# Performance work log

Measured on AMD Instinct MI355X. Metric: run time of the kernel, lower is better.

Reference implementation:

```python
import math
import jax, jax.numpy as jnp
import numpy as np

B, S, E, A, H, L, V = 4, 1024, 1024, 64, 16, 2, 32000
EPS = 1e-5
SCALE = math.sqrt(E)  # torch code scales by sqrt(input_dim) = sqrt(embedding_dim)
W_INIT_SCALE = 0.05   # torch.rand is U[0,1); scaled down for numerically sane softmax


def setup_inputs() -> dict:
    key = jax.random.key(0)
    ks = jax.random.split(key, 6)
    return {
        "x": jax.random.randint(ks[0], (B, S), 0, V),
        "emb": jax.random.normal(ks[1], (V, E), dtype=jnp.float32) * 0.02,
        "ln_gamma": jnp.ones((L, E), dtype=jnp.float32),
        "ln_beta": jnp.zeros((L, E), dtype=jnp.float32),
        "Wq": jax.random.uniform(ks[2], (L, H, A, E), dtype=jnp.float32) * W_INIT_SCALE,
        "Wk": jax.random.uniform(ks[3], (L, H, A, E), dtype=jnp.float32) * W_INIT_SCALE,
        "Wv": jax.random.uniform(ks[4], (L, H, E, E), dtype=jnp.float32) * W_INIT_SCALE,
    }


def _attn_layer(h, gamma, beta, wq, wk, wv):
    # h: [B,H,S,E]; LayerNorm over last dim (biased variance, like torch)
    mu = jnp.mean(h, axis=-1, keepdims=True)
    var = jnp.mean(jnp.square(h - mu), axis=-1, keepdims=True)
    hn = (h - mu) * jax.lax.rsqrt(var + EPS) * gamma + beta
    q = jnp.einsum('bhse,hae->bhsa', hn, wq)   # [B,H,S,A]
    k = jnp.einsum('bhse,hae->bhsa', hn, wk)   # [B,H,S,A]
    v = jnp.einsum('bhse,hoe->bhso', hn, wv)   # [B,H,S,E]
    scores = jnp.einsum('bhsa,bhta->bhst', q, k) / SCALE  # [B,H,S,S]
    w = jax.nn.softmax(scores, axis=-1)
    return jnp.einsum('bhst,bhto->bhso', w, v)  # [B,H,S,E]


def reference(x, emb, ln_gamma, ln_beta, Wq, Wk, Wv):
    # embed then replicate across heads: [B,S,E] -> [B,H,S,E]
    h = jnp.broadcast_to(emb[x][:, None, :, :], (B, H, S, E))
    for l in range(L):
        h = _attn_layer(h, ln_gamma[l], ln_beta[l], Wq[l], Wk[l], Wv[l])
    return h
```

## Files before the change

### kernel.cpp

```cpp
#include <hip/hip_runtime.h>

#define B_ 4
#define S_ 1024
#define E_ 1024
#define A_ 64
#define H_ 16
#define L_ 2

static constexpr float LN_EPS = 1e-5f;
static constexpr float INV_SCALE = 1.0f / 32.0f;

typedef __attribute__((ext_vector_type(8))) short bf16x8;
typedef __attribute__((ext_vector_type(4))) float f32x4;

__device__ __forceinline__ unsigned short f2bf(float f) {
  unsigned u = __float_as_uint(f);
  u += 0x7fffu + ((u >> 16) & 1u);
  return (unsigned short)(u >> 16);
}
__device__ __forceinline__ float bf2f(unsigned short s) {
  return __uint_as_float(((unsigned)s) << 16);
}

__device__ __forceinline__ float block_sum256(float v, float* red) {
#pragma unroll
  for (int o = 32; o > 0; o >>= 1) v += __shfl_down(v, o, 64);
  const int lane = threadIdx.x & 63;
  const int w = threadIdx.x >> 6;
  if (lane == 0) red[w] = v;
  __syncthreads();
  if (threadIdx.x == 0) red[0] = red[0] + red[1] + red[2] + red[3];
  __syncthreads();
  float r = red[0];
  __syncthreads();
  return r;
}

__device__ __forceinline__ float block_max256(float v, float* red) {
#pragma unroll
  for (int o = 32; o > 0; o >>= 1) v = fmaxf(v, __shfl_down(v, o, 64));
  const int lane = threadIdx.x & 63;
  const int w = threadIdx.x >> 6;
  if (lane == 0) red[w] = v;
  __syncthreads();
  if (threadIdx.x == 0) red[0] = fmaxf(fmaxf(red[0], red[1]), fmaxf(red[2], red[3]));
  __syncthreads();
  float r = red[0];
  __syncthreads();
  return r;
}

__global__ __launch_bounds__(256) void cvt_f32_bf16(const float* __restrict__ in,
                                                    unsigned short* __restrict__ out, long n) {
  long i = ((long)blockIdx.x * 256 + threadIdx.x) * 4;
  const long stride = (long)gridDim.x * 1024;
  for (; i < n; i += stride) {
    float4 v = *(const float4*)(in + i);
    ushort4 o;
    o.x = f2bf(v.x); o.y = f2bf(v.y); o.z = f2bf(v.z); o.w = f2bf(v.w);
    *(ushort4*)(out + i) = o;
  }
}

__global__ __launch_bounds__(256) void cvt_qk_concat(const float* __restrict__ Wq,
                                                     const float* __restrict__ Wk,
                                                     unsigned short* __restrict__ out) {
  const long total = (long)L_ * H_ * 128 * E_;
  long i = ((long)blockIdx.x * 256 + threadIdx.x) * 4;
  const long stride = (long)gridDim.x * 1024;
  for (; i < total; i += stride) {
    const long e = i % E_;
    const long rowhe = i / E_;
    const int row = (int)(rowhe % 128);
    const long lh = rowhe / 128;
    const float* src = (row < 64 ? Wq : Wk) + (lh * 64 + (row & 63)) * E_ + e;
    float4 v = *(const float4*)src;
    ushort4 o;
    o.x = f2bf(v.x); o.y = f2bf(v.y); o.z = f2bf(v.z); o.w = f2bf(v.w);
    *(ushort4*)(out + i) = o;
  }
}

__global__ __launch_bounds__(256) void embed_ln_kernel(
    const int* __restrict__ x, const float* __restrict__ emb,
    const float* __restrict__ gamma, const float* __restrict__ beta,
    unsigned short* __restrict__ out) {
  __shared__ float red[4];
  const int row = blockIdx.x;
  const int tid = threadIdx.x;
  const float* src = emb + (long)x[row] * E_;
  float4 v = *(const float4*)(src + tid * 4);
  const float mean = block_sum256(v.x + v.y + v.z + v.w, red) * (1.f / E_);
  float dx = v.x - mean, dy = v.y - mean, dz = v.z - mean, dw = v.w - mean;
  const float var = block_sum256(dx * dx + dy * dy + dz * dz + dw * dw, red) * (1.f / E_);
  const float rstd = rsqrtf(var + LN_EPS);
  float4 g = *(const float4*)(gamma + tid * 4);
  float4 b = *(const float4*)(beta + tid * 4);
  ushort4 o;
  o.x = f2bf(dx * rstd * g.x + b.x);
  o.y = f2bf(dy * rstd * g.y + b.y);
  o.z = f2bf(dz * rstd * g.z + b.z);
  o.w = f2bf(dw * rstd * g.w + b.w);
  *(ushort4*)(out + (long)row * E_ + tid * 4) = o;
}

__global__ __launch_bounds__(256) void ln_bf16_kernel(
    const unsigned short* __restrict__ h, const float* __restrict__ gamma,
    const float* __restrict__ beta, unsigned short* __restrict__ out) {
  __shared__ float red[4];
  const long row = blockIdx.x;
  const int tid = threadIdx.x;
  ushort4 raw = *(const ushort4*)(h + row * (long)E_ + tid * 4);
  float vx = bf2f(raw.x), vy = bf2f(raw.y), vz = bf2f(raw.z), vw = bf2f(raw.w);
  const float mean = block_sum256(vx + vy + vz + vw, red) * (1.f / E_);
  float dx = vx - mean, dy = vy - mean, dz = vz - mean, dw = vw - mean;
  const float var = block_sum256(dx * dx + dy * dy + dz * dz + dw * dw, red) * (1.f / E_);
  const float rstd = rsqrtf(var + LN_EPS);
  float4 g = *(const float4*)(gamma + tid * 4);
  float4 b = *(const float4*)(beta + tid * 4);
  ushort4 o;
  o.x = f2bf(dx * rstd * g.x + b.x);
  o.y = f2bf(dy * rstd * g.y + b.y);
  o.z = f2bf(dz * rstd * g.z + b.z);
  o.w = f2bf(dw * rstd * g.w + b.w);
  *(ushort4*)(out + row * E_ + tid * 4) = o;
}

__global__ __launch_bounds__(256) void softmax_bf16_kernel(unsigned short* __restrict__ sc) {
  __shared__ float red[4];
  unsigned short* p = sc + (long)blockIdx.x * S_;
  const int tid = threadIdx.x;
  ushort4 raw = *(const ushort4*)(p + tid * 4);
  float v0 = bf2f(raw.x), v1 = bf2f(raw.y), v2 = bf2f(raw.z), v3 = bf2f(raw.w);
  float m = block_max256(fmaxf(fmaxf(v0, v1), fmaxf(v2, v3)), red);
  v0 = __expf(v0 - m); v1 = __expf(v1 - m); v2 = __expf(v2 - m); v3 = __expf(v3 - m);
  const float s = block_sum256(v0 + v1 + v2 + v3, red);
  const float inv = 1.f / s;
  ushort4 o;
  o.x = f2bf(v0 * inv); o.y = f2bf(v1 * inv); o.z = f2bf(v2 * inv); o.w = f2bf(v3 * inv);
  *(ushort4*)(p + tid * 4) = o;
}

__device__ __forceinline__ void gload_lds16(const void* g, void* l) {
  __builtin_amdgcn_global_load_lds((const __attribute__((address_space(1))) void*)g,
                                   (__attribute__((address_space(3))) void*)l, 16, 0, 0);
}

template <int ROWS>
__device__ __forceinline__ void stage_tile(const unsigned short* __restrict__ src, int ldRow,
                                           unsigned short* lds, int tid) {
  const int rb = tid >> 3;
  const int gslot = (tid & 7) ^ (rb & 7);
  const int wbase = (tid >> 6) * 512;
#pragma unroll
  for (int i = 0; i < ROWS / 32; ++i) {
    const unsigned short* g = src + (long)(i * 32 + rb) * ldRow + gslot * 8;
    gload_lds16(g, lds + i * 2048 + wbase);
  }
}

__device__ __forceinline__ bf16x8 lds_frag(const unsigned short* base, int r, int slot) {
  const int byteoff = (r << 7) + ((slot ^ (r & 7)) << 4);
  return *(const bf16x8*)((const char*)base + byteoff);
}

template <int BM, int BN, bool OUT_BF16>
__global__ __launch_bounds__(256) void mfma_gemm_nt(
    const unsigned short* __restrict__ Aall, const unsigned short* __restrict__ Ball,
    void* __restrict__ Call, int M, int N, int K, int lda, int ldb,
    long aSB, long aSH, long bSB, long bSH, int Hn, float alpha) {
  __shared__ unsigned short As[BM * 64];
  __shared__ unsigned short Bs[BN * 64];
  const int batch = blockIdx.z;
  const int bb = batch / Hn, hh = batch % Hn;
  const unsigned short* Ap = Aall + (long)bb * aSB + (long)hh * aSH;
  const unsigned short* Bp = Ball + (long)bb * bSB + (long)hh * bSH;
  const int tid = threadIdx.x;
  const int lane = tid & 63;
  const int wave = tid >> 6;
  const int wr = wave >> 1, wc = wave & 1;
  const int bm = blockIdx.x * BM, bn = blockIdx.y * BN;
  constexpr int FM = BM / 32, FN = BN / 32;

  f32x4 acc[FM][FN];
#pragma unroll
  for (int i = 0; i < FM; ++i)
#pragma unroll
    for (int j = 0; j < FN; ++j) acc[i][j] = (f32x4)(0.f);

  for (int k0 = 0; k0 < K; k0 += 64) {
    stage_tile<BM>(Ap + (long)bm * lda + k0, lda, As, tid);
    stage_tile<BN>(Bp + (long)bn * ldb + k0, ldb, Bs, tid);
    __syncthreads();
#pragma unroll
    for (int kb = 0; kb < 2; ++kb) {
      const int slot = (kb << 2) + (lane >> 4);
      bf16x8 af[FM], bfv[FN];
#pragma unroll
      for (int mi = 0; mi < FM; ++mi)
        af[mi] = lds_frag(As, wr * (BM / 2) + mi * 16 + (lane & 15), slot);
#pragma unroll
      for (int ni = 0; ni < FN; ++ni)
        bfv[ni] = lds_frag(Bs, wc * (BN / 2) + ni * 16 + (lane & 15), slot);
#pragma unroll
      for (int mi = 0; mi < FM; ++mi)
#pragma unroll
        for (int ni = 0; ni < FN; ++ni)
          acc[mi][ni] = __builtin_amdgcn_mfma_f32_16x16x32_bf16(af[mi], bfv[ni], acc[mi][ni], 0, 0, 0);
    }
    __syncthreads();
  }

#pragma unroll
  for (int mi = 0; mi < FM; ++mi) {
    const int row = bm + wr * (BM / 2) + mi * 16 + ((lane >> 4) << 2);
#pragma unroll
    for (int ni = 0; ni < FN; ++ni) {
      const int col = bn + wc * (BN / 2) + ni * 16 + (lane & 15);
#pragma unroll
      for (int r = 0; r < 4; ++r) {
        const float v = acc[mi][ni][r] * alpha;
        const long idx = (long)batch * M * N + (long)(row + r) * N + col;
        if constexpr (OUT_BF16)
          ((unsigned short*)Call)[idx] = f2bf(v);
        else
          ((float*)Call)[idx] = v;
      }
    }
  }
}

__device__ __forceinline__ void stage_unit256(const unsigned short* __restrict__ src, int ldRow,
                                              char* lds_unit, int tid) {
#pragma unroll
  for (int i = 0; i < 2; ++i) {
    const int r = i * 128 + (tid >> 2);
    const int sg = (tid & 3) ^ ((r >> 1) & 3);
    const unsigned short* g = src + (long)r * ldRow + sg * 8;
    gload_lds16(g, lds_unit + i * 8192 + ((tid >> 6) << 10));
  }
}

__device__ __forceinline__ bf16x8 lds_frag256(const char* opbase, int kh, int r, int ss) {
  return *(const bf16x8*)(opbase + kh * 16384 + r * 64 + ((ss ^ ((r >> 1) & 3)) << 4));
}

template <bool OUT_BF16>
__global__ __launch_bounds__(512, 2) void mfma_gemm256_nt(
    const unsigned short* __restrict__ Aall, const unsigned short* __restrict__ Ball,
    void* __restrict__ Call, int M, int N, int K, int lda, int ldb,
    long aSB, long aSH, long bSB, long bSH, int Hn, float alpha) {
  extern __shared__ char lds[];
  const int nx = gridDim.x, ny = gridDim.y;
  const int nwg = nx * ny * gridDim.z;
  int f = blockIdx.x + nx * (blockIdx.y + ny * blockIdx.z);
  if ((nwg & 7) == 0) f = (f & 7) * (nwg >> 3) + (f >> 3);
  const int bx = f % nx;
  const int by = (f / nx) % ny;
  const int batch = f / (nx * ny);

  const int bb = batch / Hn, hh = batch % Hn;
  const unsigned short* Ap = Aall + (long)bb * aSB + (long)hh * aSH + (long)bx * 256 * lda;
  const unsigned short* Bp = Ball + (long)bb * bSB + (long)hh * bSH + (long)by * 256 * ldb;
  const int tid = threadIdx.x;
  const int lane = tid & 63;
  const int w = tid >> 6;
  const int wr = w >> 2, wc = w & 3;

  f32x4 acc[8][4];
#pragma unroll
  for (int i = 0; i < 8; ++i)
#pragma unroll
    for (int j = 0; j < 4; ++j) acc[i][j] = (f32x4)(0.f);

  const int NT = K >> 6;
  stage_unit256(Ap, lda, lds, tid);
  stage_unit256(Bp, ldb, lds + 32768, tid);
  stage_unit256(Ap + 32, lda, lds + 16384, tid);
  stage_unit256(Bp + 32, ldb, lds + 32768 + 16384, tid);
  asm volatile("s_waitcnt vmcnt(0)\n\ts_barrier" ::: "memory");

  for (int t = 0; t < NT; ++t) {
    const char* cur = lds + (t & 1) * 65536;
    char* nxt = lds + ((t + 1) & 1) * 65536;
    const unsigned short* An = Ap + (long)(t + 1) * 64;
    const unsigned short* Bn = Bp + (long)(t + 1) * 64;
    const bool pf = (t + 1 < NT);
#pragma unroll
    for (int kh = 0; kh < 2; ++kh) {
      bf16x8 a[8], b[4];
      const int ss = lane >> 4;
#pragma unroll
      for (int mi = 0; mi < 8; ++mi)
        a[mi] = lds_frag256(cur, kh, wr * 128 + mi * 16 + (lane & 15), ss);
#pragma unroll
      for (int ni = 0; ni < 4; ++ni)
        b[ni] = lds_frag256(cur + 32768, kh, wc * 64 + ni * 16 + (lane & 15), ss);
      if (pf) {
        stage_unit256(An + kh * 32, lda, nxt + kh * 16384, tid);
        stage_unit256(Bn + kh * 32, ldb, nxt + 32768 + kh * 16384, tid);
      }
      asm volatile("s_barrier" ::: "memory");
      __builtin_amdgcn_s_setprio(1);
#pragma unroll
      for (int mi = 0; mi < 8; ++mi)
#pragma unroll
        for (int ni = 0; ni < 4; ++ni)
          acc[mi][ni] = __builtin_amdgcn_mfma_f32_16x16x32_bf16(a[mi], b[ni], acc[mi][ni], 0, 0, 0);
      __builtin_amdgcn_s_setprio(0);
      asm volatile("s_waitcnt vmcnt(4)\n\ts_barrier" ::: "memory");
    }
  }

#pragma unroll
  for (int mi = 0; mi < 8; ++mi) {
    const int row0 = bx * 256 + wr * 128 + mi * 16 + ((lane >> 4) << 2);
#pragma unroll
    for (int ni = 0; ni < 4; ++ni) {
      const int col = by * 256 + wc * 64 + ni * 16 + (lane & 15);
#pragma unroll
      for (int r = 0; r < 4; ++r) {
        const float v = acc[mi][ni][r] * alpha;
        const long idx = (long)batch * M * N + (long)(row0 + r) * N + col;
        if constexpr (OUT_BF16)
          ((unsigned short*)Call)[idx] = f2bf(v);
        else
          ((float*)Call)[idx] = v;
      }
    }
  }
}

extern "C" void kernel_launch(void* const* d_in, const int* in_sizes, int n_in,
                              void* d_out, int out_size, void* d_ws, size_t ws_size,
                              hipStream_t stream) {
  const int* x = (const int*)d_in[0];
  const float* emb = (const float*)d_in[1];
  const float* gamma = (const float*)d_in[2];
  const float* beta = (const float*)d_in[3];
  const float* Wq = (const float*)d_in[4];
  const float* Wk = (const float*)d_in[5];
  const float* Wv = (const float*)d_in[6];
  float* out = (float*)d_out;

  (void)hipFuncSetAttribute(reinterpret_cast<const void*>(&mfma_gemm256_nt<true>),
                            hipFuncAttributeMaxDynamicSharedMemorySize, 131072);
  (void)hipFuncSetAttribute(reinterpret_cast<const void*>(&mfma_gemm256_nt<false>),
                            hipFuncAttributeMaxDynamicSharedMemorySize, 131072);

  const long WQK_N = (long)L_ * H_ * 128 * E_;
  const long WV_N = (long)L_ * H_ * E_ * E_;
  const long HN_N = (long)B_ * H_ * S_ * E_;
  const long QK_N = (long)B_ * H_ * S_ * 128;
  unsigned short* wqk = (unsigned short*)d_ws;
  unsigned short* wv_bf = wqk + WQK_N;
  unsigned short* hn = wv_bf + WV_N;
  unsigned short* qk = hn + HN_N;
  unsigned short* v_t = qk + QK_N;
  unsigned short* sc = v_t + HN_N;
  unsigned short* hid0 = (unsigned short*)d_out;

  const dim3 blk(256), blk512(512);
  const dim3 grid256(4, 4, 64);
  cvt_qk_concat<<<2048, blk, 0, stream>>>(Wq, Wk, wqk);
  cvt_f32_bf16<<<4096, blk, 0, stream>>>(Wv, wv_bf, WV_N);

  for (int l = 0; l < L_; ++l) {
    long hSB, hSH;
    if (l == 0) {
      embed_ln_kernel<<<B_ * S_, blk, 0, stream>>>(x, emb, gamma, beta, hn);
      hSB = (long)S_ * E_; hSH = 0;
    } else {
      ln_bf16_kernel<<<B_ * H_ * S_, blk, 0, stream>>>(
          hid0, gamma + (long)l * E_, beta + (long)l * E_, hn);
      hSB = (long)H_ * S_ * E_; hSH = (long)S_ * E_;
    }
    mfma_gemm_nt<128, 128, true><<<dim3(8, 1, 64), blk, 0, stream>>>(
        hn, wqk + (long)l * H_ * 128 * E_, qk, S_, 128, E_, E_, E_,
        hSB, hSH, 0L, (long)128 * E_, H_, 1.f);
    mfma_gemm256_nt<true><<<grid256, blk512, 131072, stream>>>(
        wv_bf + (long)l * H_ * E_ * E_, hn, v_t, E_, S_, E_, E_, E_,
        0L, (long)E_ * E_, hSB, hSH, H_, 1.f);
    mfma_gemm_nt<128, 128, true><<<dim3(8, 8, 64), blk, 0, stream>>>(
        qk, qk + 64, sc, S_, S_, 64, 128, 128,
        (long)H_ * S_ * 128, (long)S_ * 128, (long)H_ * S_ * 128, (long)S_ * 128, H_, INV_SCALE);
    softmax_bf16_kernel<<<B_ * H_ * S_, blk, 0, stream>>>(sc);
    if (l == 0) {
      mfma_gemm256_nt<true><<<grid256, blk512, 131072, stream>>>(
          sc, v_t, hid0, S_, E_, S_, S_, S_,
          (long)H_ * S_ * S_, (long)S_ * S_, (long)H_ * E_ * S_, (long)E_ * S_, H_, 1.f);
    } else {
      mfma_gemm256_nt<false><<<grid256, blk512, 131072, stream>>>(
          sc, v_t, out, S_, E_, S_, S_, S_,
          (long)H_ * S_ * S_, (long)S_ * S_, (long)H_ * E_ * S_, (long)E_ * S_, H_, 1.f);
    }
  }
}
```

Baseline: 1.017 ms.

## Fuse QK^T scores with softmax and simplify 256-tile GEMM pipeline

Replaces the separate scores GEMM and row-softmax kernels with a single kernel. Each block loads 64 query rows and all 1024 keys into LDS, computes scores with MFMA, and does the row max/sum reductions in registers and LDS before writing normalized bf16 probabilities. This avoids writing and re-reading the unnormalized score matrix and drops one launch. Separately, the 256-tile GEMM drops the explicit (512,2) occupancy hint, the setprio calls and the per-half partial waitcnt. It now prefetches the whole next K tile up front and syncs once per iteration, which may reduce overlap of loads with compute.

```diff
diff --git a/kernel.cpp b/kernel.cpp
--- a/kernel.cpp
+++ b/kernel.cpp
@@ -30,20 +30,6 @@
   if (lane == 0) red[w] = v;
   __syncthreads();
   if (threadIdx.x == 0) red[0] = red[0] + red[1] + red[2] + red[3];
-  __syncthreads();
-  float r = red[0];
-  __syncthreads();
-  return r;
-}
-
-__device__ __forceinline__ float block_max256(float v, float* red) {
-#pragma unroll
-  for (int o = 32; o > 0; o >>= 1) v = fmaxf(v, __shfl_down(v, o, 64));
-  const int lane = threadIdx.x & 63;
-  const int w = threadIdx.x >> 6;
-  if (lane == 0) red[w] = v;
-  __syncthreads();
-  if (threadIdx.x == 0) red[0] = fmaxf(fmaxf(red[0], red[1]), fmaxf(red[2], red[3]));
   __syncthreads();
   float r = red[0];
   __syncthreads();
@@ -126,21 +112,6 @@
   *(ushort4*)(out + row * E_ + tid * 4) = o;
 }
 
-__global__ __launch_bounds__(256) void softmax_bf16_kernel(unsigned short* __restrict__ sc) {
-  __shared__ float red[4];
-  unsigned short* p = sc + (long)blockIdx.x * S_;
-  const int tid = threadIdx.x;
-  ushort4 raw = *(const ushort4*)(p + tid * 4);
-  float v0 = bf2f(raw.x), v1 = bf2f(raw.y), v2 = bf2f(raw.z), v3 = bf2f(raw.w);
-  float m = block_max256(fmaxf(fmaxf(v0, v1), fmaxf(v2, v3)), red);
-  v0 = __expf(v0 - m); v1 = __expf(v1 - m); v2 = __expf(v2 - m); v3 = __expf(v3 - m);
-  const float s = block_sum256(v0 + v1 + v2 + v3, red);
-  const float inv = 1.f / s;
-  ushort4 o;
-  o.x = f2bf(v0 * inv); o.y = f2bf(v1 * inv); o.z = f2bf(v2 * inv); o.w = f2bf(v3 * inv);
-  *(ushort4*)(p + tid * 4) = o;
-}
-
 __device__ __forceinline__ void gload_lds16(const void* g, void* l) {
   __builtin_amdgcn_global_load_lds((const __attribute__((address_space(1))) void*)g,
                                    (__attribute__((address_space(3))) void*)l, 16, 0, 0);
@@ -246,7 +217,7 @@
 }
 
 template <bool OUT_BF16>
-__global__ __launch_bounds__(512, 2) void mfma_gemm256_nt(
+__global__ __launch_bounds__(512) void mfma_gemm256_nt(
     const unsigned short* __restrict__ Aall, const unsigned short* __restrict__ Ball,
     void* __restrict__ Call, int M, int N, int K, int lda, int ldb,
     long aSB, long aSH, long bSB, long bSH, int Hn, float alpha) {
@@ -266,6 +237,8 @@
   const int lane = tid & 63;
   const int w = tid >> 6;
   const int wr = w >> 2, wc = w & 3;
+  const int ss = lane >> 4;
+  const int ar = lane & 15;
 
   f32x4 acc[8][4];
 #pragma unroll
@@ -275,41 +248,38 @@
 
   const int NT = K >> 6;
   stage_unit256(Ap, lda, lds, tid);
+  stage_unit256(Ap + 32, lda, lds + 16384, tid);
   stage_unit256(Bp, ldb, lds + 32768, tid);
-  stage_unit256(Ap + 32, lda, lds + 16384, tid);
-  stage_unit256(Bp + 32, ldb, lds + 32768 + 16384, tid);
-  asm volatile("s_waitcnt vmcnt(0)\n\ts_barrier" ::: "memory");
+  stage_unit256(Bp + 32, ldb, lds + 49152, tid);
+  __syncthreads();
 
   for (int t = 0; t < NT; ++t) {
     const char* cur = lds + (t & 1) * 65536;
     char* nxt = lds + ((t + 1) & 1) * 65536;
-    const unsigned short* An = Ap + (long)(t + 1) * 64;
-    const unsigned short* Bn = Bp + (long)(t + 1) * 64;
-    const bool pf = (t + 1 < NT);
+    if (t + 1 < NT) {
+      const unsigned short* An = Ap + (long)(t + 1) * 64;
+      const unsigned short* Bn = Bp + (long)(t + 1) * 64;
+      stage_unit256(An, lda, nxt, tid);
+      stage_unit256(An + 32, lda, nxt + 16384, tid);
+      stage_unit256(Bn, ldb, nxt + 32768, tid);
+      stage_unit256(Bn + 32, ldb, nxt + 49152, tid);
+    }
 #pragma unroll
     for (int kh = 0; kh < 2; ++kh) {
-      bf16x8 a[8], b[4];
-      const int ss = lane >> 4;
+      bf16x8 b[4], a[8];
+#pragma unroll
+      for (int ni = 0; ni < 4; ++ni)
+        b[ni] = lds_frag256(cur + 32768, kh, wc * 64 + ni * 16 + ar, ss);
 #pragma unroll
       for (int mi = 0; mi < 8; ++mi)
-        a[mi] = lds_frag256(cur, kh, wr * 128 + mi * 16 + (lane & 15), ss);
-#pragma unroll
-      for (int ni = 0; ni < 4; ++ni)
-        b[ni] = lds_frag256(cur + 32768, kh, wc * 64 + ni * 16 + (lane & 15), ss);
-      if (pf) {
-        stage_unit256(An + kh * 32, lda, nxt + kh * 16384, tid);
-        stage_unit256(Bn + kh * 32, ldb, nxt + 32768 + kh * 16384, tid);
-      }
-      asm volatile("s_barrier" ::: "memory");
-      __builtin_amdgcn_s_setprio(1);
+        a[mi] = lds_frag256(cur, kh, wr * 128 + mi * 16 + ar, ss);
 #pragma unroll
       for (int mi = 0; mi < 8; ++mi)
 #pragma unroll
         for (int ni = 0; ni < 4; ++ni)
           acc[mi][ni] = __builtin_amdgcn_mfma_f32_16x16x32_bf16(a[mi], b[ni], acc[mi][ni], 0, 0, 0);
-      __builtin_amdgcn_s_setprio(0);
-      asm volatile("s_waitcnt vmcnt(4)\n\ts_barrier" ::: "memory");
-    }
+    }
+    __syncthreads();
   }
 
 #pragma unroll
@@ -329,6 +299,131 @@
       }
     }
   }
+}
+
+__global__ __launch_bounds__(512) void scores_softmax_kernel(
+    const unsigned short* __restrict__ qk, unsigned short* __restrict__ sc) {
+  extern __shared__ char smem[];
+  unsigned short* q_lds = (unsigned short*)smem;
+  unsigned short* k_lds = (unsigned short*)(smem + 8192);
+  float* redm = (float*)(smem + 8192 + 131072);
+  float* reds = redm + 512;
+
+  const int tid = threadIdx.x;
+  const int lane = tid & 63;
+  const int w = tid >> 6;
+  const int batch = blockIdx.z;
+  const int bm = blockIdx.x * 64;
+  const unsigned short* qbase = qk + (long)batch * S_ * 128 + (long)bm * 128;
+  const unsigned short* kbase = qk + (long)batch * S_ * 128 + 64;
+
+  {
+    const int r = tid >> 3;
+    const int slot = (tid & 7) ^ (r & 7);
+    gload_lds16(qbase + (long)r * 128 + slot * 8, (char*)q_lds + w * 1024);
+  }
+#pragma unroll
+  for (int p = 0; p < 16; ++p) {
+    const int r = p * 64 + (tid >> 3);
+    const int slot = (tid & 7) ^ (r & 7);
+    gload_lds16(kbase + (long)r * 128 + slot * 8, (char*)k_lds + p * 8192 + w * 1024);
+  }
+  __syncthreads();
+
+  const int ss = lane >> 4, ar = lane & 15;
+  f32x4 acc[4][8];
+#pragma unroll
+  for (int i = 0; i < 4; ++i)
+#pragma unroll
+    for (int j = 0; j < 8; ++j) acc[i][j] = (f32x4)(0.f);
+
+#pragma unroll
+  for (int kh = 0; kh < 2; ++kh) {
+    bf16x8 a[4];
+#pragma unroll
+    for (int mi = 0; mi < 4; ++mi)
+      a[mi] = lds_frag(q_lds, mi * 16 + ar, kh * 4 + ss);
+#pragma unroll
+    for (int ni = 0; ni < 8; ++ni) {
+      bf16x8 bv = lds_frag(k_lds, w * 128 + ni * 16 + ar, kh * 4 + ss);
+#pragma unroll
+      for (int mi = 0; mi < 4; ++mi)
+        acc[mi][ni] = __builtin_amdgcn_mfma_f32_16x16x32_bf16(a[mi], bv, acc[mi][ni], 0, 0, 0);
+    }
+  }
+
+#pragma unroll
+  for (int mi = 0; mi < 4; ++mi)
+#pragma unroll
+    for (int ni = 0; ni < 8; ++ni)
+#pragma unroll
+      for (int r = 0; r < 4; ++r) acc[mi][ni][r] *= INV_SCALE;
+
+  float gmax[4][4];
+#pragma unroll
+  for (int mi = 0; mi < 4; ++mi)
+#pragma unroll
+    for (int r = 0; r < 4; ++r) {
+      float m = acc[mi][0][r];
+#pragma unroll
+      for (int ni = 1; ni < 8; ++ni) m = fmaxf(m, acc[mi][ni][r]);
+#pragma unroll
+      for (int mask = 1; mask < 16; mask <<= 1) m = fmaxf(m, __shfl_xor(m, mask, 64));
+      if ((lane & 15) == 0) redm[(mi * 16 + (lane >> 4) * 4 + r) * 8 + w] = m;
+      gmax[mi][r] = m;
+    }
+  __syncthreads();
+#pragma unroll
+  for (int mi = 0; mi < 4; ++mi)
+#pragma unroll
+    for (int r = 0; r < 4; ++r) {
+      const int row = mi * 16 + (lane >> 4) * 4 + r;
+      float g = redm[row * 8];
+#pragma unroll
+      for (int w2 = 1; w2 < 8; ++w2) g = fmaxf(g, redm[row * 8 + w2]);
+      gmax[mi][r] = g;
+    }
+
+  float ginv[4][4];
+#pragma unroll
+  for (int mi = 0; mi < 4; ++mi)
+#pragma unroll
+    for (int r = 0; r < 4; ++r) {
+      float s = 0.f;
+#pragma unroll
+      for (int ni = 0; ni < 8; ++ni) {
+        const float e = __expf(acc[mi][ni][r] - gmax[mi][r]);
+        acc[mi][ni][r] = e;
+        s += e;
+      }
+#pragma unroll
+      for (int mask = 1; mask < 16; mask <<= 1) s += __shfl_xor(s, mask, 64);
+      if ((lane & 15) == 0) reds[(mi * 16 + (lane >> 4) * 4 + r) * 8 + w] = s;
+    }
+  __syncthreads();
+#pragma unroll
+  for (int mi = 0; mi < 4; ++mi)
+#pragma unroll
+    for (int r = 0; r < 4; ++r) {
+      const int row = mi * 16 + (lane >> 4) * 4 + r;
+      float g = 0.f;
+#pragma unroll
+      for (int w2 = 0; w2 < 8; ++w2) g += reds[row * 8 + w2];
+      ginv[mi][r] = 1.f / g;
+    }
+
+  unsigned short* out = sc + (long)batch * S_ * S_;
+#pragma unroll
+  for (int mi = 0; mi < 4; ++mi)
+#pragma unroll
+    for (int r = 0; r < 4; ++r) {
+      const long row = bm + mi * 16 + (lane >> 4) * 4 + r;
+#pragma unroll
+      for (int ni = 0; ni < 8; ++ni) {
+        const int col = w * 128 + ni * 16 + ar;
+        out[row * S_ + col] = f2bf(acc[mi][ni][r] * ginv[mi][r]);
+      }
+    }
 }
 
 extern "C" void kernel_launch(void* const* d_in, const int* in_sizes, int n_in,
@@ -347,6 +442,8 @@
                             hipFuncAttributeMaxDynamicSharedMemorySize, 131072);
   (void)hipFuncSetAttribute(reinterpret_cast<const void*>(&mfma_gemm256_nt<false>),
                             hipFuncAttributeMaxDynamicSharedMemorySize, 131072);
+  (void)hipFuncSetAttribute(reinterpret_cast<const void*>(&scores_softmax_kernel),
+                            hipFuncAttributeMaxDynamicSharedMemorySize, 143360);
 
   const long WQK_N = (long)L_ * H_ * 128 * E_;
   const long WV_N = (long)L_ * H_ * E_ * E_;
@@ -381,10 +478,7 @@
     mfma_gemm256_nt<true><<<grid256, blk512, 131072, stream>>>(
         wv_bf + (long)l * H_ * E_ * E_, hn, v_t, E_, S_, E_, E_, E_,
         0L, (long)E_ * E_, hSB, hSH, H_, 1.f);
-    mfma_gemm_nt<128, 128, true><<<dim3(8, 8, 64), blk, 0, stream>>>(
-        qk, qk + 64, sc, S_, S_, 64, 128, 128,
-        (long)H_ * S_ * 128, (long)S_ * 128, (long)H_ * S_ * 128, (long)S_ * 128, H_, INV_SCALE);
-    softmax_bf16_kernel<<<B_ * H_ * S_, blk, 0, stream>>>(sc);
+    scores_softmax_kernel<<<dim3(16, 1, 64), blk512, 143360, stream>>>(qk, sc);
     if (l == 0) {
       mfma_gemm256_nt<true><<<grid256, blk512, 131072, stream>>>(
           sc, v_t, hid0, S_, E_, S_, S_, S_,
```

New measurement: 1.031 ms. No clear change (+1.4%).
